# Kernel optimization log

Measured on AMD Instinct MI355X. Metric: run time of the kernel, lower is better.

The kernel has to match this reference:

```python
import jax, jax.numpy as jnp
import numpy as np

DIM_MODEL = 512
KDIM = 64
NUM_FREQS = 70


def setup_inputs() -> dict:
    key = jax.random.key(0)
    ks = jax.random.split(key, 8)
    B, N = 8, 2048
    src = jax.random.normal(ks[0], (B, N, DIM_MODEL), dtype=jnp.float32)
    bias_tensor = jax.random.normal(ks[1], (N, N, 4), dtype=jnp.float32)
    multiplier = jax.random.uniform(ks[2], (B, N, N), dtype=jnp.float32)
    # f_theta_lc params
    W_r = jax.random.normal(ks[3], (NUM_FREQS, 2), dtype=jnp.float32)  # std=1.0 init
    C = jnp.ones((NUM_FREQS,), dtype=jnp.float32)
    log_p = jnp.float32(0.0)
    # Xavier-uniform attention projections (torch Linear weight layout [out, in])
    lim = float(np.sqrt(6.0 / (DIM_MODEL + KDIM)))
    W_q = jax.random.uniform(ks[4], (KDIM, DIM_MODEL), minval=-lim, maxval=lim, dtype=jnp.float32)
    W_k = jax.random.uniform(ks[5], (KDIM, DIM_MODEL), minval=-lim, maxval=lim, dtype=jnp.float32)
    W_v = jax.random.uniform(ks[6], (KDIM, DIM_MODEL), minval=-lim, maxval=lim, dtype=jnp.float32)
    s = jnp.float32(1.0)
    return {"src": src, "bias_tensor": bias_tensor, "multiplier": multiplier,
            "W_r": W_r, "C": C, "log_p": log_p,
            "W_q": W_q, "W_k": W_k, "W_v": W_v, "s": s}


def _f_theta(bias_tensor, W_r, C, log_p):
    # bias_tensor: [N, N, 4]; W_r: [F, 2]
    k1 = jnp.einsum('nmi,fi->nmf', bias_tensor[:, :, 0:2], W_r)
    k2 = jnp.einsum('nmi,fi->nmf', bias_tensor[:, :, 2:4], W_r)
    diff = jnp.cos(k1) + jnp.sin(k1) - jnp.cos(k2) - jnp.sin(k2)
    sigma = jnp.abs(jnp.sum(diff * C, axis=-1))  # [N, N]
    p = jnp.clip(jnp.exp(log_p), 0.5, 3.0)
    return jnp.exp(-jnp.power(sigma + 1e-6, p))


def reference(src, bias_tensor, multiplier, W_r, C, log_p, W_q, W_k, W_v, s):
    B = _f_theta(bias_tensor, W_r, C, log_p)  # [N, N]
    Q = jnp.einsum('bnd,kd->bnk', src, W_q)
    K = jnp.einsum('bnd,kd->bnk', src, W_k)
    V = jnp.einsum('bnd,kd->bnk', src, W_v)
    denom = jnp.sqrt(jnp.float32(KDIM))
    logits = (jnp.einsum('bnk,bmk->bnm', Q, K) + B[None]) / denom
    logits = logits * (s * multiplier)
    attn = jax.nn.softmax(logits, axis=-1)
    return jnp.einsum('bnm,bmk->bnk', attn, V)
```

## Files before the change

### kernel.cpp

```cpp
#include <hip/hip_runtime.h>
#include <hip/hip_bf16.h>

#define N_SEQ 2048
#define NB 8
#define DM 512
#define KD 64
#define NF 70

#define TG 512
#define TRANGE 6.5f
#define TSCL (511.0f / 13.0f)
#define TOFS (6.5f * TSCL)

typedef float f32x4 __attribute__((ext_vector_type(4)));
typedef short v8s  __attribute__((ext_vector_type(8)));

__device__ __forceinline__ ushort f2bf(float x) {
    uint u = __float_as_uint(x);
    return (ushort)((u + 0x7FFFu + ((u >> 16) & 1u)) >> 16);
}
__device__ __forceinline__ float bf2f(ushort h) {
    return __uint_as_float(((uint)h) << 16);
}
__device__ __forceinline__ uint cvtpk(float lo, float hi) {
    uint r;
    asm("v_cvt_pk_bf16_f32 %0, %1, %2" : "=v"(r) : "v"(lo), "v"(hi));
    return r;
}

__global__ __launch_bounds__(256) void tbuild_kernel(
    const float* __restrict__ Wr, const float* __restrict__ Cc,
    float* __restrict__ Tg)
{
    const float SQ2 = 1.41421356237309504880f;
    const float R2PI = 0.15915494309189533577f;
    int idx = blockIdx.x * 256 + threadIdx.x;
    int j = idx >> 9, i = idx & (TG - 1);
    const float h = 2.0f * TRANGE / (TG - 1);
    float y = -TRANGE + j * h;
    float x = -TRANGE + i * h;
    float g = 0.f;
    for (int f = 0; f < NF; ++f) {
        float w0 = Wr[2*f] * R2PI, w1 = Wr[2*f+1] * R2PI, cf = Cc[f];
        float k = __builtin_amdgcn_fractf(fmaf(x, w0, fmaf(y, w1, 0.125f)));
        g = fmaf(cf, __builtin_amdgcn_sinf(k), g);
    }
    Tg[idx] = g * SQ2;
}

__global__ __launch_bounds__(256) void tpack_kernel(
    const float* __restrict__ Tg, float4* __restrict__ T4)
{
    int idx = blockIdx.x * 256 + threadIdx.x;
    int j = idx >> 9, i = idx & (TG - 1);
    int i1 = min(i + 1, TG - 1);
    int j1 = min(j + 1, TG - 1);
    float4 q;
    q.x = Tg[j*TG + i];
    q.y = Tg[j*TG + i1];
    q.z = Tg[j1*TG + i];
    q.w = Tg[j1*TG + i1];
    T4[idx] = q;
}

__device__ __forceinline__ float tlookup(const float4* __restrict__ T4,
                                         float x, float y)
{
    float u = fmaf(x, TSCL, TOFS);
    float v = fmaf(y, TSCL, TOFS);
    u = fminf(fmaxf(u, 0.0f), 510.999f);
    v = fminf(fmaxf(v, 0.0f), 510.999f);
    int iu = (int)u, iv = (int)v;
    float fu = __builtin_amdgcn_fractf(u);
    float fv = __builtin_amdgcn_fractf(v);
    float4 q = T4[iv * TG + iu];
    float t0 = fmaf(fu, q.y - q.x, q.x);
    float t1 = fmaf(fu, q.w - q.z, q.z);
    return fmaf(fv, t1 - t0, t0);
}

__global__ __launch_bounds__(256) void ftheta_kernel(
    const float* __restrict__ bias, const float4* __restrict__ T4,
    const float* __restrict__ logp, ushort* __restrict__ Bm)
{
    int tid = threadIdx.x;
    long i0 = (long)blockIdx.x * 512 + tid;
    long i1 = i0 + 256;
    float4 a = ((const float4*)bias)[i0];
    float4 b = ((const float4*)bias)[i1];
    float gA1 = tlookup(T4, a.x, a.y);
    float gA2 = tlookup(T4, a.z, a.w);
    float gB1 = tlookup(T4, b.x, b.y);
    float gB2 = tlookup(T4, b.z, b.w);
    float s0 = fabsf(gA1 - gA2) + 1e-6f;
    float s1 = fabsf(gB1 - gB2) + 1e-6f;
    float p = __expf(logp[0]);
    p = fminf(fmaxf(p, 0.5f), 3.0f);
    if (p == 1.0f) {
        Bm[i0] = f2bf(__expf(-s0));
        Bm[i1] = f2bf(__expf(-s1));
    } else {
        Bm[i0] = f2bf(__expf(-__powf(s0, p)));
        Bm[i1] = f2bf(__expf(-__powf(s1, p)));
    }
}

__global__ __launch_bounds__(256) void qkv_kernel(
    const float* __restrict__ src, const float* __restrict__ Wq,
    const float* __restrict__ Wk, const float* __restrict__ Wv,
    ushort* __restrict__ Qh, ushort* __restrict__ Ql,
    ushort* __restrict__ Kh, ushort* __restrict__ VhT)
{
    __shared__ ushort sS[32][72];
    __shared__ ushort sW[192][72];
    int tid = threadIdx.x;
    int lane = tid & 63, w = tid >> 6;
    int wr = w >> 1, wc = w & 1;
    int g = lane >> 4, ln = lane & 15;
    int row0 = blockIdx.x * 32;

    f32x4 acc[6];
#pragma unroll
    for (int t = 0; t < 6; ++t) acc[t] = {0.f, 0.f, 0.f, 0.f};

    for (int kc = 0; kc < 8; ++kc) {
        int k0 = kc * 64;
        __syncthreads();
        {
            int r = tid >> 3, c8 = (tid & 7) * 8;
            float4 f0 = *(const float4*)&src[(long)(row0 + r)*DM + k0 + c8];
            float4 f1 = *(const float4*)&src[(long)(row0 + r)*DM + k0 + c8 + 4];
            uint4 pk = make_uint4(cvtpk(f0.x, f0.y), cvtpk(f0.z, f0.w),
                                  cvtpk(f1.x, f1.y), cvtpk(f1.z, f1.w));
            *(uint4*)&sS[r][c8] = pk;
        }
        {
#pragma unroll
            for (int j = 0; j < 6; ++j) {
                int slot = tid + j*256;
                int r = slot >> 3, c8 = (slot & 7) * 8;
                const float* Wp = (r < 64) ? Wq : (r < 128 ? Wk : Wv);
                int rr = r & 63;
                float4 f0 = *(const float4*)&Wp[(long)rr*DM + k0 + c8];
                float4 f1 = *(const float4*)&Wp[(long)rr*DM + k0 + c8 + 4];
                uint4 pk = make_uint4(cvtpk(f0.x, f0.y), cvtpk(f0.z, f0.w),
                                      cvtpk(f1.x, f1.y), cvtpk(f1.z, f1.w));
                *(uint4*)&sW[r][c8] = pk;
            }
        }
        __syncthreads();
#pragma unroll
        for (int kw = 0; kw < 2; ++kw) {
            v8s bsrc = *(const v8s*)&sS[16*wr + ln][32*kw + 8*g];
#pragma unroll
            for (int t = 0; t < 6; ++t) {
                v8s aw = *(const v8s*)&sW[96*wc + 16*t + ln][32*kw + 8*g];
                acc[t] = __builtin_amdgcn_mfma_f32_16x16x32_bf16(aw, bsrc, acc[t], 0, 0, 0);
            }
        }
    }
    int n = row0 + 16*wr + ln;
    int bb = n >> 11, nn = n & 2047;
#pragma unroll
    for (int t = 0; t < 6; ++t) {
        int c0 = 96*wc + 16*t + 4*g;
        f32x4 v = acc[t];
        uint2 hp = make_uint2(cvtpk(v[0], v[1]), cvtpk(v[2], v[3]));
        if (c0 < 64) {
            *(uint2*)&Qh[(long)n*KD + c0] = hp;
            float h0 = __uint_as_float(hp.x << 16);
            float h1 = __uint_as_float(hp.x & 0xFFFF0000u);
            float h2 = __uint_as_float(hp.y << 16);
            float h3 = __uint_as_float(hp.y & 0xFFFF0000u);
            uint2 lp = make_uint2(cvtpk(v[0]-h0, v[1]-h1), cvtpk(v[2]-h2, v[3]-h3));
            *(uint2*)&Ql[(long)n*KD + c0] = lp;
        } else if (c0 < 128) {
            *(uint2*)&Kh[(long)n*KD + (c0 - 64)] = hp;
        } else {
            int kv = c0 - 128;
            VhT[((long)bb*KD + kv + 0)*N_SEQ + nn] = (ushort)(hp.x & 0xFFFFu);
            VhT[((long)bb*KD + kv + 1)*N_SEQ + nn] = (ushort)(hp.x >> 16);
            VhT[((long)bb*KD + kv + 2)*N_SEQ + nn] = (ushort)(hp.y & 0xFFFFu);
            VhT[((long)bb*KD + kv + 3)*N_SEQ + nn] = (ushort)(hp.y >> 16);
        }
    }
}

__global__ __launch_bounds__(256, 4) void attn_mfma_kernel(
    const ushort* __restrict__ Qh, const ushort* __restrict__ Ql,
    const ushort* __restrict__ Kh, const ushort* __restrict__ VhT,
    const ushort* __restrict__ Bm, const float* __restrict__ mult,
    const float* __restrict__ sp,
    ushort* __restrict__ Opart, float* __restrict__ Mp, float* __restrict__ Lp)
{
    __shared__ ushort sKh[64][72];
    __shared__ ushort sVT[64][72];
    __shared__ ushort sP[4][16][72];

    int tid = threadIdx.x;
    int lane = tid & 63, w = tid >> 6;
    int g = lane >> 4, ln = lane & 15;
    int bid = blockIdx.x;
    int b = bid & 7, rest = bid >> 3, p = rest & 3, nt = rest >> 2;
    int n0 = nt * 64;

    int qrow = n0 + w*16 + ln;
    long qoff = ((long)b*N_SEQ + qrow)*KD + 8*g;
    v8s qh0 = *(const v8s*)&Qh[qoff];
    v8s qh1 = *(const v8s*)&Qh[qoff + 32];
    v8s ql0 = *(const v8s*)&Ql[qoff];
    v8s ql1 = *(const v8s*)&Ql[qoff + 32];

    float s  = sp[0];
    float qs = 0.125f * s;
    float M = -1e30f, L = 0.f;
    f32x4 accO[4];
#pragma unroll
    for (int i = 0; i < 4; ++i) accO[i] = {0.f, 0.f, 0.f, 0.f};

    long brow = (long)qrow * N_SEQ;
    long urow = ((long)b*N_SEQ + qrow) * N_SEQ;
    long vtb  = (long)b*KD*N_SEQ;
    long kbB  = (long)b*N_SEQ*KD;

    int srow = tid >> 3, sc8 = (tid & 7) * 8;

    uint4 rKh0, rKh1, rVT0, rVT1;
    ushort4 nBq[4]; float4 nUq[4];
    {
        int m0 = p*512;
        rKh0 = *(const uint4*)&Kh[kbB + (long)(m0+srow)*KD + sc8];
        rKh1 = *(const uint4*)&Kh[kbB + (long)(m0+srow+32)*KD + sc8];
        rVT0 = *(const uint4*)&VhT[vtb + (long)srow*N_SEQ + m0 + sc8];
        rVT1 = *(const uint4*)&VhT[vtb + (long)(srow+32)*N_SEQ + m0 + sc8];
#pragma unroll
        for (int sub = 0; sub < 4; ++sub) {
            nBq[sub] = *(const ushort4*)&Bm[brow + m0 + 16*sub + 4*g];
            nUq[sub] = *(const float4*)&mult[urow + m0 + 16*sub + 4*g];
        }
    }

    for (int mt = 0; mt < 8; ++mt) {
        int m0 = p*512 + mt*64;
        __syncthreads();
        *(uint4*)&sKh[srow][sc8]      = rKh0;
        *(uint4*)&sKh[srow + 32][sc8] = rKh1;
        *(uint4*)&sVT[srow][sc8]      = rVT0;
        *(uint4*)&sVT[srow + 32][sc8] = rVT1;
        __syncthreads();

        if (mt < 7) {
            int m1 = m0 + 64;
            rKh0 = *(const uint4*)&Kh[kbB + (long)(m1+srow)*KD + sc8];
            rKh1 = *(const uint4*)&Kh[kbB + (long)(m1+srow+32)*KD + sc8];
            rVT0 = *(const uint4*)&VhT[vtb + (long)srow*N_SEQ + m1 + sc8];
            rVT1 = *(const uint4*)&VhT[vtb + (long)(srow+32)*N_SEQ + m1 + sc8];
        }

        f32x4 S[4];
#pragma unroll
        for (int i = 0; i < 4; ++i) S[i] = {0.f, 0.f, 0.f, 0.f};
        __builtin_amdgcn_s_setprio(1);
#pragma unroll
        for (int ks = 0; ks < 2; ++ks) {
            v8s qh = ks ? qh1 : qh0;
            v8s ql = ks ? ql1 : ql0;
#pragma unroll
            for (int sub = 0; sub < 4; ++sub) {
                v8s kh = *(const v8s*)&sKh[16*sub + ln][32*ks + 8*g];
                S[sub] = __builtin_amdgcn_mfma_f32_16x16x32_bf16(kh, qh, S[sub], 0, 0, 0);
                S[sub] = __builtin_amdgcn_mfma_f32_16x16x32_bf16(kh, ql, S[sub], 0, 0, 0);
            }
        }
        __builtin_amdgcn_s_setprio(0);

        float lg[16]; float mx = -1e30f;
#pragma unroll
        for (int sub = 0; sub < 4; ++sub) {
            float b0 = bf2f(nBq[sub].x), b1 = bf2f(nBq[sub].y);
            float b2 = bf2f(nBq[sub].z), b3 = bf2f(nBq[sub].w);
            lg[4*sub+0] = (S[sub][0] + b0) * nUq[sub].x * qs;
            lg[4*sub+1] = (S[sub][1] + b1) * nUq[sub].y * qs;
            lg[4*sub+2] = (S[sub][2] + b2) * nUq[sub].z * qs;
            lg[4*sub+3] = (S[sub][3] + b3) * nUq[sub].w * qs;
            mx = fmaxf(mx, fmaxf(fmaxf(lg[4*sub+0], lg[4*sub+1]),
                                 fmaxf(lg[4*sub+2], lg[4*sub+3])));
        }
        if (mt < 7) {
            int m1 = m0 + 64;
#pragma unroll
            for (int sub = 0; sub < 4; ++sub) {
                nBq[sub] = *(const ushort4*)&Bm[brow + m1 + 16*sub + 4*g];
                nUq[sub] = *(const float4*)&mult[urow + m1 + 16*sub + 4*g];
            }
        }
        mx = fmaxf(mx, __shfl_xor(mx, 16));
        mx = fmaxf(mx, __shfl_xor(mx, 32));
        float Mn = fmaxf(M, mx);
        float sc = __expf(M - Mn);
        float ps = 0.f;
#pragma unroll
        for (int i = 0; i < 16; ++i) {
            float e = __expf(lg[i] - Mn);
            lg[i] = e; ps += e;
        }
        ps += __shfl_xor(ps, 16);
        ps += __shfl_xor(ps, 32);
        L = L * sc + ps; M = Mn;

#pragma unroll
        for (int sub = 0; sub < 4; ++sub) {
            uint2 pk = make_uint2(cvtpk(lg[4*sub+0], lg[4*sub+1]),
                                  cvtpk(lg[4*sub+2], lg[4*sub+3]));
            *(uint2*)&sP[w][ln][16*sub + 4*g] = pk;
        }

#pragma unroll
        for (int i = 0; i < 4; ++i) accO[i] *= sc;
        __builtin_amdgcn_s_setprio(1);
#pragma unroll
        for (int ks = 0; ks < 2; ++ks) {
            v8s pp = *(const v8s*)&sP[w][ln][32*ks + 8*g];
#pragma unroll
            for (int sub = 0; sub < 4; ++sub) {
                v8s vh = *(const v8s*)&sVT[16*sub + ln][32*ks + 8*g];
                accO[sub] = __builtin_amdgcn_mfma_f32_16x16x32_bf16(vh, pp, accO[sub], 0, 0, 0);
            }
        }
        __builtin_amdgcn_s_setprio(0);
    }

    long ob = ((long)bid*64 + (w*16 + ln)) * 64;
#pragma unroll
    for (int sub = 0; sub < 4; ++sub) {
        uint2 pk = make_uint2(cvtpk(accO[sub][0], accO[sub][1]),
                              cvtpk(accO[sub][2], accO[sub][3]));
        *(uint2*)&Opart[ob + 16*sub + 4*g] = pk;
    }
    if (g == 0) {
        Mp[bid*64 + w*16 + ln] = M;
        Lp[bid*64 + w*16 + ln] = L;
    }
}

__global__ __launch_bounds__(256) void combine_kernel(
    const ushort* __restrict__ Opart, const float* __restrict__ Mp,
    const float* __restrict__ Lp, float* __restrict__ out)
{
    int idx = blockIdx.x * 256 + threadIdx.x;
    int kq = idx & 15;
    int row = idx >> 4;
    int b = row >> 11, n = row & 2047;
    int nt = n >> 6, r = n & 63;
    int bid0 = ((nt*4) << 3) | b;
    float Mq[4], Lq[4];
#pragma unroll
    for (int p = 0; p < 4; ++p) {
        Mq[p] = Mp[(bid0 + 8*p)*64 + r];
        Lq[p] = Lp[(bid0 + 8*p)*64 + r];
    }
    float Mx = fmaxf(fmaxf(Mq[0], Mq[1]), fmaxf(Mq[2], Mq[3]));
    float4 acc = make_float4(0.f, 0.f, 0.f, 0.f);
    float Ls = 0.f;
#pragma unroll
    for (int p = 0; p < 4; ++p) {
        float e = __expf(Mq[p] - Mx);
        Ls += Lq[p] * e;
        ushort4 o = *(const ushort4*)&Opart[((long)(bid0 + 8*p)*64 + r)*64 + 4*kq];
        acc.x = fmaf(e, bf2f(o.x), acc.x);
        acc.y = fmaf(e, bf2f(o.y), acc.y);
        acc.z = fmaf(e, bf2f(o.z), acc.z);
        acc.w = fmaf(e, bf2f(o.w), acc.w);
    }
    float inv = 1.0f / Ls;
    float4 o;
    o.x = acc.x * inv; o.y = acc.y * inv;
    o.z = acc.z * inv; o.w = acc.w * inv;
    *(float4*)&out[(long)row*64 + 4*kq] = o;
}

extern "C" void kernel_launch(void* const* d_in, const int* in_sizes, int n_in,
                              void* d_out, int out_size, void* d_ws, size_t ws_size,
                              hipStream_t stream) {
    const float* src  = (const float*)d_in[0];
    const float* bias = (const float*)d_in[1];
    const float* mult = (const float*)d_in[2];
    const float* Wr   = (const float*)d_in[3];
    const float* Cc   = (const float*)d_in[4];
    const float* logp = (const float*)d_in[5];
    const float* Wq   = (const float*)d_in[6];
    const float* Wk   = (const float*)d_in[7];
    const float* Wv   = (const float*)d_in[8];
    const float* sp   = (const float*)d_in[9];
    float* outp = (float*)d_out;

    const size_t QKV_E = (size_t)NB * N_SEQ * KD;
    ushort* wsu = (ushort*)d_ws;
    ushort* Bm  = wsu;
    ushort* Qh  = wsu + (size_t)N_SEQ * N_SEQ;
    ushort* Ql  = Qh + QKV_E;
    ushort* Kh  = Ql + QKV_E;
    ushort* VhT = Kh + QKV_E;
    ushort* Opart = VhT + QKV_E;
    float* Mp = (float*)(Opart + (size_t)1024 * 64 * 64);
    float* Lp = Mp + (size_t)1024 * 64;
    float4* T4 = (float4*)(Lp + (size_t)1024 * 64);
    float*  Tg = (float*)(T4 + (size_t)TG * TG);

    tbuild_kernel<<<(TG*TG)/256, 256, 0, stream>>>(Wr, Cc, Tg);
    tpack_kernel<<<(TG*TG)/256, 256, 0, stream>>>(Tg, T4);
    ftheta_kernel<<<(N_SEQ*(long)N_SEQ)/512, 256, 0, stream>>>(bias, T4, logp, Bm);
    qkv_kernel<<<(NB*N_SEQ)/32, 256, 0, stream>>>(src, Wq, Wk, Wv, Qh, Ql, Kh, VhT);
    attn_mfma_kernel<<<1024, 256, 0, stream>>>(Qh, Ql, Kh, VhT, Bm, mult, sp,
                                               Opart, Mp, Lp);
    combine_kernel<<<1024, 256, 0, stream>>>(Opart, Mp, Lp, outp);
}
```

Measured before the change: 125.2 us.

## Merge QKV projection and f_theta bias kernels into one heterogeneous launch

Fuses the independent qkv projection and f_theta bias-table kernels into a single launch, with the first 512 blocks doing the QKV MFMA GEMM and the remaining 4096 blocks computing the bias. This removes one kernel launch and lets the compute-bound GEMM blocks overlap with the memory-bound bias blocks. The bias path now handles 4 elements per thread instead of 2 and issues all 8 table gathers before interpolating, for more memory-level parallelism. The cost is that the bias blocks reserve the GEMM's shared memory, which may limit occupancy.

```diff
diff --git a/kernel.cpp b/kernel.cpp
--- a/kernel.cpp
+++ b/kernel.cpp
@@ -63,125 +63,130 @@
     T4[idx] = q;
 }
 
-__device__ __forceinline__ float tlookup(const float4* __restrict__ T4,
-                                         float x, float y)
-{
-    float u = fmaf(x, TSCL, TOFS);
-    float v = fmaf(y, TSCL, TOFS);
-    u = fminf(fmaxf(u, 0.0f), 510.999f);
-    v = fminf(fmaxf(v, 0.0f), 510.999f);
-    int iu = (int)u, iv = (int)v;
-    float fu = __builtin_amdgcn_fractf(u);
-    float fv = __builtin_amdgcn_fractf(v);
-    float4 q = T4[iv * TG + iu];
-    float t0 = fmaf(fu, q.y - q.x, q.x);
-    float t1 = fmaf(fu, q.w - q.z, q.z);
-    return fmaf(fv, t1 - t0, t0);
-}
-
-__global__ __launch_bounds__(256) void ftheta_kernel(
-    const float* __restrict__ bias, const float4* __restrict__ T4,
-    const float* __restrict__ logp, ushort* __restrict__ Bm)
-{
-    int tid = threadIdx.x;
-    long i0 = (long)blockIdx.x * 512 + tid;
-    long i1 = i0 + 256;
-    float4 a = ((const float4*)bias)[i0];
-    float4 b = ((const float4*)bias)[i1];
-    float gA1 = tlookup(T4, a.x, a.y);
-    float gA2 = tlookup(T4, a.z, a.w);
-    float gB1 = tlookup(T4, b.x, b.y);
-    float gB2 = tlookup(T4, b.z, b.w);
-    float s0 = fabsf(gA1 - gA2) + 1e-6f;
-    float s1 = fabsf(gB1 - gB2) + 1e-6f;
-    float p = __expf(logp[0]);
-    p = fminf(fmaxf(p, 0.5f), 3.0f);
-    if (p == 1.0f) {
-        Bm[i0] = f2bf(__expf(-s0));
-        Bm[i1] = f2bf(__expf(-s1));
-    } else {
-        Bm[i0] = f2bf(__expf(-__powf(s0, p)));
-        Bm[i1] = f2bf(__expf(-__powf(s1, p)));
-    }
-}
-
-__global__ __launch_bounds__(256) void qkv_kernel(
+#define QKV_BLOCKS 512
+
+__global__ __launch_bounds__(256) void fat_kernel(
     const float* __restrict__ src, const float* __restrict__ Wq,
     const float* __restrict__ Wk, const float* __restrict__ Wv,
     ushort* __restrict__ Qh, ushort* __restrict__ Ql,
-    ushort* __restrict__ Kh, ushort* __restrict__ VhT)
+    ushort* __restrict__ Kh, ushort* __restrict__ VhT,
+    const float* __restrict__ bias, const float4* __restrict__ T4,
+    const float* __restrict__ logp, ushort* __restrict__ Bm)
 {
     __shared__ ushort sS[32][72];
     __shared__ ushort sW[192][72];
     int tid = threadIdx.x;
-    int lane = tid & 63, w = tid >> 6;
-    int wr = w >> 1, wc = w & 1;
-    int g = lane >> 4, ln = lane & 15;
-    int row0 = blockIdx.x * 32;
-
-    f32x4 acc[6];
-#pragma unroll
-    for (int t = 0; t < 6; ++t) acc[t] = {0.f, 0.f, 0.f, 0.f};
-
-    for (int kc = 0; kc < 8; ++kc) {
-        int k0 = kc * 64;
-        __syncthreads();
-        {
-            int r = tid >> 3, c8 = (tid & 7) * 8;
-            float4 f0 = *(const float4*)&src[(long)(row0 + r)*DM + k0 + c8];
-            float4 f1 = *(const float4*)&src[(long)(row0 + r)*DM + k0 + c8 + 4];
-            uint4 pk = make_uint4(cvtpk(f0.x, f0.y), cvtpk(f0.z, f0.w),
-                                  cvtpk(f1.x, f1.y), cvtpk(f1.z, f1.w));
-            *(uint4*)&sS[r][c8] = pk;
-        }
-        {
-#pragma unroll
-            for (int j = 0; j < 6; ++j) {
-                int slot = tid + j*256;
-                int r = slot >> 3, c8 = (slot & 7) * 8;
-                const float* Wp = (r < 64) ? Wq : (r < 128 ? Wk : Wv);
-                int rr = r & 63;
-                float4 f0 = *(const float4*)&Wp[(long)rr*DM + k0 + c8];
-                float4 f1 = *(const float4*)&Wp[(long)rr*DM + k0 + c8 + 4];
+
+    if (blockIdx.x < QKV_BLOCKS) {
+        int lane = tid & 63, w = tid >> 6;
+        int wr = w >> 1, wc = w & 1;
+        int g = lane >> 4, ln = lane & 15;
+        int row0 = blockIdx.x * 32;
+
+        f32x4 acc[6];
+#pragma unroll
+        for (int t = 0; t < 6; ++t) acc[t] = {0.f, 0.f, 0.f, 0.f};
+
+        for (int kc = 0; kc < 8; ++kc) {
+            int k0 = kc * 64;
+            __syncthreads();
+            {
+                int r = tid >> 3, c8 = (tid & 7) * 8;
+                float4 f0 = *(const float4*)&src[(long)(row0 + r)*DM + k0 + c8];
+                float4 f1 = *(const float4*)&src[(long)(row0 + r)*DM + k0 + c8 + 4];
                 uint4 pk = make_uint4(cvtpk(f0.x, f0.y), cvtpk(f0.z, f0.w),
                                       cvtpk(f1.x, f1.y), cvtpk(f1.z, f1.w));
-                *(uint4*)&sW[r][c8] = pk;
-            }
-        }
-        __syncthreads();
-#pragma unroll
-        for (int kw = 0; kw < 2; ++kw) {
-            v8s bsrc = *(const v8s*)&sS[16*wr + ln][32*kw + 8*g];
-#pragma unroll
-            for (int t = 0; t < 6; ++t) {
-                v8s aw = *(const v8s*)&sW[96*wc + 16*t + ln][32*kw + 8*g];
-                acc[t] = __builtin_amdgcn_mfma_f32_16x16x32_bf16(aw, bsrc, acc[t], 0, 0, 0);
-            }
-        }
-    }
-    int n = row0 + 16*wr + ln;
-    int bb = n >> 11, nn = n & 2047;
-#pragma unroll
-    for (int t = 0; t < 6; ++t) {
-        int c0 = 96*wc + 16*t + 4*g;
-        f32x4 v = acc[t];
-        uint2 hp = make_uint2(cvtpk(v[0], v[1]), cvtpk(v[2], v[3]));
-        if (c0 < 64) {
-            *(uint2*)&Qh[(long)n*KD + c0] = hp;
-            float h0 = __uint_as_float(hp.x << 16);
-            float h1 = __uint_as_float(hp.x & 0xFFFF0000u);
-            float h2 = __uint_as_float(hp.y << 16);
-            float h3 = __uint_as_float(hp.y & 0xFFFF0000u);
-            uint2 lp = make_uint2(cvtpk(v[0]-h0, v[1]-h1), cvtpk(v[2]-h2, v[3]-h3));
-            *(uint2*)&Ql[(long)n*KD + c0] = lp;
-        } else if (c0 < 128) {
-            *(uint2*)&Kh[(long)n*KD + (c0 - 64)] = hp;
+                *(uint4*)&sS[r][c8] = pk;
+            }
+            {
+#pragma unroll
+                for (int j = 0; j < 6; ++j) {
+                    int slot = tid + j*256;
+                    int r = slot >> 3, c8 = (slot & 7) * 8;
+                    const float* Wp = (r < 64) ? Wq : (r < 128 ? Wk : Wv);
+                    int rr = r & 63;
+                    float4 f0 = *(const float4*)&Wp[(long)rr*DM + k0 + c8];
+                    float4 f1 = *(const float4*)&Wp[(long)rr*DM + k0 + c8 + 4];
+                    uint4 pk = make_uint4(cvtpk(f0.x, f0.y), cvtpk(f0.z, f0.w),
+                                          cvtpk(f1.x, f1.y), cvtpk(f1.z, f1.w));
+                    *(uint4*)&sW[r][c8] = pk;
+                }
+            }
+            __syncthreads();
+#pragma unroll
+            for (int kw = 0; kw < 2; ++kw) {
+                v8s bsrc = *(const v8s*)&sS[16*wr + ln][32*kw + 8*g];
+#pragma unroll
+                for (int t = 0; t < 6; ++t) {
+                    v8s aw = *(const v8s*)&sW[96*wc + 16*t + ln][32*kw + 8*g];
+                    acc[t] = __builtin_amdgcn_mfma_f32_16x16x32_bf16(aw, bsrc, acc[t], 0, 0, 0);
+                }
+            }
+        }
+        int n = row0 + 16*wr + ln;
+        int bb = n >> 11, nn = n & 2047;
+#pragma unroll
+        for (int t = 0; t < 6; ++t) {
+            int c0 = 96*wc + 16*t + 4*g;
+            f32x4 v = acc[t];
+            uint2 hp = make_uint2(cvtpk(v[0], v[1]), cvtpk(v[2], v[3]));
+            if (c0 < 64) {
+                *(uint2*)&Qh[(long)n*KD + c0] = hp;
+                float h0 = __uint_as_float(hp.x << 16);
+                float h1 = __uint_as_float(hp.x & 0xFFFF0000u);
+                float h2 = __uint_as_float(hp.y << 16);
+                float h3 = __uint_as_float(hp.y & 0xFFFF0000u);
+                uint2 lp = make_uint2(cvtpk(v[0]-h0, v[1]-h1), cvtpk(v[2]-h2, v[3]-h3));
+                *(uint2*)&Ql[(long)n*KD + c0] = lp;
+            } else if (c0 < 128) {
+                *(uint2*)&Kh[(long)n*KD + (c0 - 64)] = hp;
+            } else {
+                int kv = c0 - 128;
+                VhT[((long)bb*KD + kv + 0)*N_SEQ + nn] = (ushort)(hp.x & 0xFFFFu);
+                VhT[((long)bb*KD + kv + 1)*N_SEQ + nn] = (ushort)(hp.x >> 16);
+                VhT[((long)bb*KD + kv + 2)*N_SEQ + nn] = (ushort)(hp.y & 0xFFFFu);
+                VhT[((long)bb*KD + kv + 3)*N_SEQ + nn] = (ushort)(hp.y >> 16);
+            }
+        }
+    } else {
+        long base = (long)(blockIdx.x - QKV_BLOCKS) * 1024 + tid;
+        float4 e[4];
+        e[0] = ((const float4*)bias)[base];
+        e[1] = ((const float4*)bias)[base + 256];
+        e[2] = ((const float4*)bias)[base + 512];
+        e[3] = ((const float4*)bias)[base + 768];
+
+        float fu[8], fv[8]; float4 q[8];
+#pragma unroll
+        for (int k = 0; k < 8; ++k) {
+            float x = (k & 1) ? e[k>>1].z : e[k>>1].x;
+            float y = (k & 1) ? e[k>>1].w : e[k>>1].y;
+            float u = fmaf(x, TSCL, TOFS);
+            float v = fmaf(y, TSCL, TOFS);
+            u = fminf(fmaxf(u, 0.0f), 510.999f);
+            v = fminf(fmaxf(v, 0.0f), 510.999f);
+            int iu = (int)u, iv = (int)v;
+            fu[k] = __builtin_amdgcn_fractf(u);
+            fv[k] = __builtin_amdgcn_fractf(v);
+            q[k] = T4[iv * TG + iu];
+        }
+        float gq[8];
+#pragma unroll
+        for (int k = 0; k < 8; ++k) {
+            float t0 = fmaf(fu[k], q[k].y - q[k].x, q[k].x);
+            float t1 = fmaf(fu[k], q[k].w - q[k].z, q[k].z);
+            gq[k] = fmaf(fv[k], t1 - t0, t0);
+        }
+        float p = __expf(logp[0]);
+        p = fminf(fmaxf(p, 0.5f), 3.0f);
+        if (p == 1.0f) {
+#pragma unroll
+            for (int k = 0; k < 4; ++k)
+                Bm[base + 256*k] = f2bf(__expf(-(fabsf(gq[2*k] - gq[2*k+1]) + 1e-6f)));
         } else {
-            int kv = c0 - 128;
-            VhT[((long)bb*KD + kv + 0)*N_SEQ + nn] = (ushort)(hp.x & 0xFFFFu);
-            VhT[((long)bb*KD + kv + 1)*N_SEQ + nn] = (ushort)(hp.x >> 16);
-            VhT[((long)bb*KD + kv + 2)*N_SEQ + nn] = (ushort)(hp.y & 0xFFFFu);
-            VhT[((long)bb*KD + kv + 3)*N_SEQ + nn] = (ushort)(hp.y >> 16);
+#pragma unroll
+            for (int k = 0; k < 4; ++k)
+                Bm[base + 256*k] = f2bf(__expf(-__powf(fabsf(gq[2*k] - gq[2*k+1]) + 1e-6f, p)));
         }
     }
 }
@@ -409,8 +414,8 @@
 
     tbuild_kernel<<<(TG*TG)/256, 256, 0, stream>>>(Wr, Cc, Tg);
     tpack_kernel<<<(TG*TG)/256, 256, 0, stream>>>(Tg, T4);
-    ftheta_kernel<<<(N_SEQ*(long)N_SEQ)/512, 256, 0, stream>>>(bias, T4, logp, Bm);
-    qkv_kernel<<<(NB*N_SEQ)/32, 256, 0, stream>>>(src, Wq, Wk, Wv, Qh, Ql, Kh, VhT);
+    fat_kernel<<<QKV_BLOCKS + 4096, 256, 0, stream>>>(
+        src, Wq, Wk, Wv, Qh, Ql, Kh, VhT, bias, T4, logp, Bm);
     attn_mfma_kernel<<<1024, 256, 0, stream>>>(Qh, Ql, Kh, VhT, Bm, mult, sp,
                                                Opart, Mp, Lp);
     combine_kernel<<<1024, 256, 0, stream>>>(Opart, Mp, Lp, outp);
```

After: 108.1 us. 1.16x faster.
